# Performance work log

Measured on AMD Instinct MI355X. Metric: run time of the kernel, lower is better.

The kernel has to match this reference:

```python
import jax, jax.numpy as jnp
import numpy as np

B, L_TEXT, N_TOKEN = 8, 2048, 2048
C_TEXT, C_OUT = 3584, 384
C_HID = C_OUT * 2
CHAIN_TYPES = (1, 2)   # heavy, light
CDR_TYPES = (2, 4, 6)  # CDR1/2/3


def setup_inputs() -> dict:
    key = jax.random.key(0)
    ks = jax.random.split(key, 10)
    text_conditioning = jax.random.normal(ks[0], (B, L_TEXT, C_TEXT), jnp.float32)
    text_mask = jnp.ones((B, L_TEXT), jnp.int32)
    chain_type_ids = jax.random.randint(ks[1], (B, L_TEXT), 0, 3).astype(jnp.int32)
    cdr_region_type_ids = jax.random.randint(ks[2], (B, L_TEXT), 0, 10).astype(jnp.int32)
    boltz_chain_type = jax.random.randint(ks[3], (B, N_TOKEN), 0, 4).astype(jnp.int32)
    boltz_region_type = jax.random.randint(ks[4], (B, N_TOKEN), 0, 10).astype(jnp.int32)
    W1 = jax.random.normal(ks[5], (C_HID, C_TEXT), jnp.float32) * 0.02
    b1 = jnp.zeros((C_HID,), jnp.float32)
    W2 = jax.random.normal(ks[6], (C_OUT, C_HID), jnp.float32) * 0.02
    b2 = jnp.zeros((C_OUT,), jnp.float32)
    scale = jnp.ones((1,), jnp.float32)
    return {
        "text_conditioning": text_conditioning, "text_mask": text_mask,
        "chain_type_ids": chain_type_ids, "cdr_region_type_ids": cdr_region_type_ids,
        "boltz_chain_type": boltz_chain_type, "boltz_region_type": boltz_region_type,
        "W1": W1, "b1": b1, "W2": W2, "b2": b2, "scale": scale,
    }


def _align_one(text_proj, tmask, pmask):
    # text_proj: [L, C]; tmask: [L] bool (text CDR positions); pmask: [N] bool (protein CDR positions)
    # The k-th masked text token (in sequence order) maps to the k-th masked protein token,
    # for k < min(n_text, n_protein). Other protein positions get zeros.
    L = tmask.shape[0]
    trank = jnp.cumsum(tmask) - 1          # rank among text CDR tokens
    n_text = jnp.sum(tmask)
    prank = jnp.cumsum(pmask) - 1          # rank among protein CDR tokens
    # idx_by_rank[r] = text index whose rank is r; out-of-range scatter indices dropped
    idx_by_rank = jnp.zeros((L,), jnp.int32).at[jnp.where(tmask, trank, L)].set(
        jnp.arange(L, dtype=jnp.int32), mode="drop")
    valid = pmask & (prank < n_text)       # prank < n_protein holds by construction under pmask
    src = idx_by_rank[jnp.clip(prank, 0, L - 1)]
    emb = text_proj[src]                   # [N, C]
    return jnp.where(valid[:, None], emb, jnp.zeros((), text_proj.dtype))


def reference(text_conditioning, text_mask, chain_type_ids, cdr_region_type_ids,
              boltz_chain_type, boltz_region_type, W1, b1, W2, b2, scale):
    # 2-layer MLP projection: c_text -> 2*c_out -> c_out with SiLU
    h = jax.nn.silu(jnp.einsum("blt,ht->blh", text_conditioning, W1) + b1)
    text_proj = jnp.einsum("blh,ch->blc", h, W2) + b2    # [B, L, C_OUT]

    tm = text_mask.astype(bool)
    result = jnp.zeros((text_conditioning.shape[0], boltz_chain_type.shape[1], W2.shape[0]),
                       text_proj.dtype)
    align = jax.vmap(_align_one)
    for ct in CHAIN_TYPES:
        for rt in CDR_TYPES:
            tmask = (chain_type_ids == ct) & (cdr_region_type_ids == rt) & tm
            pmask = (boltz_chain_type == ct) & (boltz_region_type == rt)
            # (chain, cdr) pairs write to disjoint protein positions, so add is exact
            result = result + align(text_proj, tmask, pmask)
    return scale * result
```

## Files before the change

### kernel.cpp

```cpp
#include <hip/hip_runtime.h>
#include <hip/hip_bf16.h>
#include <math.h>

typedef __bf16 bf16_t;
typedef bf16_t bf16x8 __attribute__((ext_vector_type(8)));
typedef bf16_t bf16x4 __attribute__((ext_vector_type(4)));
typedef float f32x4 __attribute__((ext_vector_type(4)));

#define L_TEXT 2048
#define N_TOKEN 2048
#define C_TEXT 3584
#define C_OUT 384
#define C_HID 768
#define BATCH 8
#define MAXROWS (BATCH * N_TOKEN)
#define PM 3072
#define NPAIR (BATCH * 6)
#define KSPLIT 4
#define KCHUNK (C_TEXT / KSPLIT)

#define NW1 (C_HID * C_TEXT / 8)
#define NW2 (C_OUT * C_HID / 8)
#define NZERO (MAXROWS * C_OUT / 4)
#define CHUNKS_TOTAL (NW1 + NW2 + NZERO)
#define CHUNK_BLOCKS (CHUNKS_TOTAL / 256)
#define GCH (C_TEXT / 8)

__global__ __launch_bounds__(64) void scan_kernel(
    const int* __restrict__ tm, const int* __restrict__ ctid,
    const int* __restrict__ cdrid, const int* __restrict__ bct,
    const int* __restrict__ brt,
    int* __restrict__ trowL, int* __restrict__ pidxL, int* __restrict__ vcnt) {
    const int bp = blockIdx.x;
    const int lane = threadIdx.x;
    const int b = bp / 6, p = bp % 6;
    const int ct = (p < 3) ? 1 : 2;
    const int rt = 2 + 2 * (p % 3);
    const unsigned long long ltm = (1ull << lane) - 1ull;

    unsigned int tbits = 0, pbits = 0;
#pragma unroll
    for (int i = 0; i < 32; i++) {
        int l = i * 64 + lane;
        unsigned int m = (ctid[b * L_TEXT + l] == ct) &&
                         (cdrid[b * L_TEXT + l] == rt) &&
                         (tm[b * L_TEXT + l] != 0);
        tbits |= m << i;
    }
#pragma unroll
    for (int i = 0; i < 32; i++) {
        int n = i * 64 + lane;
        unsigned int m = (bct[b * N_TOKEN + n] == ct) &&
                         (brt[b * N_TOKEN + n] == rt);
        pbits |= m << i;
    }
    int base = 0;
#pragma unroll
    for (int i = 0; i < 32; i++) {
        bool m = (tbits >> i) & 1;
        unsigned long long bal = __ballot(m);
        if (m) trowL[bp * L_TEXT + base + __popcll(bal & ltm)] = i * 64 + lane;
        base += __popcll(bal);
    }
    const int n_text = base;
    base = 0;
#pragma unroll
    for (int i = 0; i < 32; i++) {
        bool m = (pbits >> i) & 1;
        unsigned long long bal = __ballot(m);
        if (m) pidxL[bp * L_TEXT + base + __popcll(bal & ltm)] = i * 64 + lane;
        base += __popcll(bal);
    }
    const int n_prot = base;
    if (lane == 0) vcnt[bp] = n_text < n_prot ? n_text : n_prot;
}

__global__ __launch_bounds__(256) void prep_kernel(
    const float* __restrict__ W1, const float* __restrict__ W2,
    bf16_t* __restrict__ W1b, bf16_t* __restrict__ W2b,
    float* __restrict__ outp,
    const float* __restrict__ X,
    const int* __restrict__ trowL, const int* __restrict__ pidxL,
    const int* __restrict__ vcnt,
    int* __restrict__ rows_dst, int* __restrict__ count,
    bf16_t* __restrict__ Xg) {
    const int t = threadIdx.x;
    if (blockIdx.x < CHUNK_BLOCKS) {
        int idx = blockIdx.x * 256 + t;
        if (idx < NW1) {
            int i = idx * 8;
            float4 v0 = *(const float4*)(W1 + i);
            float4 v1 = *(const float4*)(W1 + i + 4);
            bf16x8 o;
            o[0] = (bf16_t)v0.x; o[1] = (bf16_t)v0.y; o[2] = (bf16_t)v0.z; o[3] = (bf16_t)v0.w;
            o[4] = (bf16_t)v1.x; o[5] = (bf16_t)v1.y; o[6] = (bf16_t)v1.z; o[7] = (bf16_t)v1.w;
            *(bf16x8*)(W1b + i) = o;
        } else if (idx < NW1 + NW2) {
            int i = (idx - NW1) * 8;
            float4 v0 = *(const float4*)(W2 + i);
            float4 v1 = *(const float4*)(W2 + i + 4);
            bf16x8 o;
            o[0] = (bf16_t)v0.x; o[1] = (bf16_t)v0.y; o[2] = (bf16_t)v0.z; o[3] = (bf16_t)v0.w;
            o[4] = (bf16_t)v1.x; o[5] = (bf16_t)v1.y; o[6] = (bf16_t)v1.z; o[7] = (bf16_t)v1.w;
            *(bf16x8*)(W2b + i) = o;
        } else {
            int z = idx - NW1 - NW2;
            f32x4 zv = (f32x4){0.f, 0.f, 0.f, 0.f};
            *(f32x4*)(outp + (size_t)z * 4) = zv;
        }
        return;
    }

    __shared__ int vc[NPAIR];
    const int m = blockIdx.x - CHUNK_BLOCKS;
    if (t < NPAIR) vc[t] = vcnt[t];
    __syncthreads();

    int base = 0, bp = -1, total = 0;
    for (int q = 0; q < NPAIR; q++) {
        int v = vc[q];
        if (bp < 0 && m < base + v) bp = q;
        if (bp < 0) base += v;
        total += v;
    }
    if (m == 0 && t == 0) *count = total < PM ? total : PM;
    if (bp < 0 || m >= PM) return;
    const int r = m - base;
    const int b = bp / 6;

    if (t == 0) rows_dst[m] = b * N_TOKEN + pidxL[bp * L_TEXT + r];

    const int src = b * L_TEXT + trowL[bp * L_TEXT + r];
    const float* s = X + (size_t)src * C_TEXT;
    bf16_t* d = Xg + (size_t)m * C_TEXT;
    for (int c = t; c < GCH; c += 256) {
        int i = c * 8;
        float4 v0 = *(const float4*)(s + i);
        float4 v1 = *(const float4*)(s + i + 4);
        bf16x8 o;
        o[0] = (bf16_t)v0.x; o[1] = (bf16_t)v0.y; o[2] = (bf16_t)v0.z; o[3] = (bf16_t)v0.w;
        o[4] = (bf16_t)v1.x; o[5] = (bf16_t)v1.y; o[6] = (bf16_t)v1.z; o[7] = (bf16_t)v1.w;
        *(bf16x8*)(d + i) = o;
    }
}

__global__ __launch_bounds__(256) void gemm1_kernel(
    const bf16_t* __restrict__ Xg, const bf16_t* __restrict__ W1b,
    const int* __restrict__ countp, float* __restrict__ P) {
    int count = *countp; if (count > PM) count = PM;
    const int m0 = blockIdx.x * 128;
    if (m0 >= count) return;
    const int n0 = blockIdx.y * 128;
    const int kbeg = blockIdx.z * KCHUNK;

    __shared__ __align__(16) bf16_t As[2][128][40];
    __shared__ __align__(16) bf16_t Bs[2][128][40];

    const int t = threadIdx.x;
    const int lane = t & 63;
    const int w = t >> 6;
    const int wr = w >> 1, wc = w & 1;
    const int fr = lane & 15;
    const int kq = (lane >> 4) * 8;

    f32x4 acc[4][4];
#pragma unroll
    for (int i = 0; i < 4; i++)
#pragma unroll
        for (int j = 0; j < 4; j++) acc[i][j] = (f32x4){0.f, 0.f, 0.f, 0.f};

    const bf16_t* ap[2];
    const bf16_t* bp[2];
    int ofs[2];
#pragma unroll
    for (int j = 0; j < 2; j++) {
        int c = t + 256 * j;
        int row = c >> 2, c8 = (c & 3) * 8;
        ap[j] = Xg + (size_t)(m0 + row) * C_TEXT + kbeg + c8;
        bp[j] = W1b + (size_t)(n0 + row) * C_TEXT + kbeg + c8;
        ofs[j] = row * 40 + c8;
    }

    bf16_t* AsF = &As[0][0][0];
    bf16_t* BsF = &Bs[0][0][0];
    const int BUF = 128 * 40;

    bf16x8 ra[2], rb[2];
#pragma unroll
    for (int j = 0; j < 2; j++) { ra[j] = *(const bf16x8*)(ap[j]); rb[j] = *(const bf16x8*)(bp[j]); }

    const int T = KCHUNK / 32;
    for (int tile = 0; tile < T; ++tile) {
        const int cur = tile & 1;
#pragma unroll
        for (int j = 0; j < 2; j++) {
            *(bf16x8*)(AsF + cur * BUF + ofs[j]) = ra[j];
            *(bf16x8*)(BsF + cur * BUF + ofs[j]) = rb[j];
        }
        bf16x8 na[2], nb[2];
        bool more = (tile + 1 < T);
        if (more) {
            int k = (tile + 1) * 32;
#pragma unroll
            for (int j = 0; j < 2; j++) {
                na[j] = *(const bf16x8*)(ap[j] + k);
                nb[j] = *(const bf16x8*)(bp[j] + k);
            }
        }
        __syncthreads();
        bf16x8 af[4], bfr[4];
#pragma unroll
        for (int mi = 0; mi < 4; mi++)
            af[mi] = *(const bf16x8*)(AsF + cur * BUF + (wr * 64 + mi * 16 + fr) * 40 + kq);
#pragma unroll
        for (int ni = 0; ni < 4; ni++)
            bfr[ni] = *(const bf16x8*)(BsF + cur * BUF + (wc * 64 + ni * 16 + fr) * 40 + kq);
#pragma unroll
        for (int mi = 0; mi < 4; mi++)
#pragma unroll
            for (int ni = 0; ni < 4; ni++)
                acc[mi][ni] = __builtin_amdgcn_mfma_f32_16x16x32_bf16(
                    af[mi], bfr[ni], acc[mi][ni], 0, 0, 0);
        if (more) {
#pragma unroll
            for (int j = 0; j < 2; j++) { ra[j] = na[j]; rb[j] = nb[j]; }
        }
    }

    float* Pk = P + (size_t)blockIdx.z * PM * C_HID;
    const int rj = (lane >> 4) * 4;
#pragma unroll
    for (int mi = 0; mi < 4; mi++) {
#pragma unroll
        for (int ni = 0; ni < 4; ni++) {
            int gn = n0 + wc * 64 + ni * 16 + fr;
#pragma unroll
            for (int j = 0; j < 4; j++) {
                int gm = m0 + wr * 64 + mi * 16 + rj + j;
                if (gm < count) Pk[(size_t)gm * C_HID + gn] = acc[mi][ni][j];
            }
        }
    }
}

__global__ __launch_bounds__(256) void reduce1_kernel(
    const float* __restrict__ P, const float* __restrict__ b1,
    const int* __restrict__ countp, bf16_t* __restrict__ H) {
    int count = *countp; if (count > PM) count = PM;
    int idx = blockIdx.x * 256 + threadIdx.x;
    int m = idx / (C_HID / 4);
    int c = (idx % (C_HID / 4)) * 4;
    if (m >= count) return;
    f32x4 s = *(const f32x4*)(P + (size_t)m * C_HID + c);
#pragma unroll
    for (int ks = 1; ks < KSPLIT; ks++)
        s += *(const f32x4*)(P + ((size_t)ks * PM + m) * C_HID + c);
    f32x4 bb = *(const f32x4*)(b1 + c);
    bf16x4 o;
#pragma unroll
    for (int j = 0; j < 4; j++) {
        float v = s[j] + bb[j];
        o[j] = (bf16_t)(v / (1.0f + __expf(-v)));
    }
    *(bf16x4*)(H + (size_t)m * C_HID + c) = o;
}

__global__ __launch_bounds__(256) void gemm2_kernel(
    const bf16_t* __restrict__ Hm, const bf16_t* __restrict__ W2b,
    const float* __restrict__ b2, const int* __restrict__ rows_dst,
    const int* __restrict__ countp, const float* __restrict__ scale,
    float* __restrict__ outp) {
    int count = *countp; if (count > PM) count = PM;
    const int m0 = blockIdx.x * 32;
    if (m0 >= count) return;
    const int n0 = blockIdx.y * 128;

    __shared__ __align__(16) bf16_t As[2][32][40];
    __shared__ __align__(16) bf16_t Bs[2][128][40];

    const int t = threadIdx.x;
    const int lane = t & 63;
    const int w = t >> 6;
    const int fr = lane & 15;
    const int kq = (lane >> 4) * 8;

    f32x4 acc[2][2];
#pragma unroll
    for (int i = 0; i < 2; i++)
#pragma unroll
        for (int j = 0; j < 2; j++) acc[i][j] = (f32x4){0.f, 0.f, 0.f, 0.f};

    const int arow = t >> 2, ac8 = (t & 3) * 8;
    const bool astage = (t < 128);
    const bf16_t* ap = Hm + (size_t)(m0 + arow) * C_HID + ac8;
    const int aofs = arow * 40 + ac8;
    const bf16_t* bp[2];
    int bofs[2];
#pragma unroll
    for (int j = 0; j < 2; j++) {
        int c = t + 256 * j;
        int row = c >> 2, c8 = (c & 3) * 8;
        bp[j] = W2b + (size_t)(n0 + row) * C_HID + c8;
        bofs[j] = row * 40 + c8;
    }

    bf16_t* AsF = &As[0][0][0];
    bf16_t* BsF = &Bs[0][0][0];
    const int ABUF = 32 * 40, BBUF = 128 * 40;

    bf16x8 ra;
    if (astage) ra = *(const bf16x8*)(ap);
    bf16x8 rb0 = *(const bf16x8*)(bp[0]);
    bf16x8 rb1 = *(const bf16x8*)(bp[1]);

    const int T = C_HID / 32;
    for (int tile = 0; tile < T; ++tile) {
        const int cur = tile & 1;
        if (astage) *(bf16x8*)(AsF + cur * ABUF + aofs) = ra;
        *(bf16x8*)(BsF + cur * BBUF + bofs[0]) = rb0;
        *(bf16x8*)(BsF + cur * BBUF + bofs[1]) = rb1;
        bf16x8 na, nb0, nb1;
        bool more = (tile + 1 < T);
        if (more) {
            int k = (tile + 1) * 32;
            if (astage) na = *(const bf16x8*)(ap + k);
            nb0 = *(const bf16x8*)(bp[0] + k);
            nb1 = *(const bf16x8*)(bp[1] + k);
        }
        __syncthreads();
        bf16x8 af[2], bfr[2];
#pragma unroll
        for (int mi = 0; mi < 2; mi++)
            af[mi] = *(const bf16x8*)(AsF + cur * ABUF + (mi * 16 + fr) * 40 + kq);
#pragma unroll
        for (int ni = 0; ni < 2; ni++)
            bfr[ni] = *(const bf16x8*)(BsF + cur * BBUF + (w * 32 + ni * 16 + fr) * 40 + kq);
#pragma unroll
        for (int mi = 0; mi < 2; mi++)
#pragma unroll
            for (int ni = 0; ni < 2; ni++)
                acc[mi][ni] = __builtin_amdgcn_mfma_f32_16x16x32_bf16(
                    af[mi], bfr[ni], acc[mi][ni], 0, 0, 0);
        if (more) { if (astage) ra = na; rb0 = nb0; rb1 = nb1; }
        __syncthreads();
    }

    const float sc = scale[0];
    const int rj = (lane >> 4) * 4;
#pragma unroll
    for (int mi = 0; mi < 2; mi++) {
#pragma unroll
        for (int ni = 0; ni < 2; ni++) {
            int gn = n0 + w * 32 + ni * 16 + fr;
            float bias = b2[gn];
#pragma unroll
            for (int j = 0; j < 4; j++) {
                int gm = m0 + mi * 16 + rj + j;
                if (gm < count) {
                    int dst = rows_dst[gm];
                    outp[(size_t)dst * C_OUT + gn] = sc * (acc[mi][ni][j] + bias);
                }
            }
        }
    }
}

extern "C" void kernel_launch(void* const* d_in, const int* in_sizes, int n_in,
                              void* d_out, int out_size, void* d_ws, size_t ws_size,
                              hipStream_t stream) {
    const float* X     = (const float*)d_in[0];
    const int*   tm    = (const int*)d_in[1];
    const int*   ctid  = (const int*)d_in[2];
    const int*   cdrid = (const int*)d_in[3];
    const int*   bct   = (const int*)d_in[4];
    const int*   brt   = (const int*)d_in[5];
    const float* W1    = (const float*)d_in[6];
    const float* b1    = (const float*)d_in[7];
    const float* W2    = (const float*)d_in[8];
    const float* b2    = (const float*)d_in[9];
    const float* scale = (const float*)d_in[10];

    char* ws = (char*)d_ws;
    size_t off = 0;
    int* count = (int*)(ws + off);        off += 1024;
    int* vcnt = (int*)(ws + off);         off += 1024;
    int* rows_dst = (int*)(ws + off);     off += (size_t)PM * 4;
    int* trowL = (int*)(ws + off);        off += (size_t)NPAIR * L_TEXT * 4;
    int* pidxL = (int*)(ws + off);        off += (size_t)NPAIR * L_TEXT * 4;
    bf16_t* W1b = (bf16_t*)(ws + off);    off += (size_t)C_HID * C_TEXT * 2;
    bf16_t* W2b = (bf16_t*)(ws + off);    off += (size_t)C_OUT * C_HID * 2;
    bf16_t* Xg = (bf16_t*)(ws + off);     off += (size_t)PM * C_TEXT * 2;
    bf16_t* H = (bf16_t*)(ws + off);      off += (size_t)PM * C_HID * 2;
    float* P = (float*)(ws + off);        off += (size_t)KSPLIT * PM * C_HID * 4;
    float* outp = (float*)d_out;

    scan_kernel<<<NPAIR, 64, 0, stream>>>(tm, ctid, cdrid, bct, brt,
                                          trowL, pidxL, vcnt);

    prep_kernel<<<CHUNK_BLOCKS + PM, 256, 0, stream>>>(
        W1, W2, W1b, W2b, outp, X, trowL, pidxL, vcnt, rows_dst, count, Xg);

    dim3 g1(PM / 128, C_HID / 128, KSPLIT);
    gemm1_kernel<<<g1, 256, 0, stream>>>(Xg, W1b, count, P);

    reduce1_kernel<<<(PM * C_HID / 4) / 256, 256, 0, stream>>>(P, b1, count, H);

    dim3 g2(PM / 32, C_OUT / 128);
    gemm2_kernel<<<g2, 256, 0, stream>>>(H, W2b, b2, rows_dst, count, scale, outp);
}
```

Measured before the change: 124.0 us.

## Shrink gemm1 M-tile to 32 rows and halve K-split

```diff
diff --git a/kernel.cpp b/kernel.cpp
--- a/kernel.cpp
+++ b/kernel.cpp
@@ -16,7 +16,7 @@
 #define MAXROWS (BATCH * N_TOKEN)
 #define PM 3072
 #define NPAIR (BATCH * 6)
-#define KSPLIT 4
+#define KSPLIT 2
 #define KCHUNK (C_TEXT / KSPLIT)
 
 #define NW1 (C_HID * C_TEXT / 8)
@@ -148,95 +148,91 @@
     const bf16_t* __restrict__ Xg, const bf16_t* __restrict__ W1b,
     const int* __restrict__ countp, float* __restrict__ P) {
     int count = *countp; if (count > PM) count = PM;
-    const int m0 = blockIdx.x * 128;
+    const int m0 = blockIdx.x * 32;
     if (m0 >= count) return;
     const int n0 = blockIdx.y * 128;
     const int kbeg = blockIdx.z * KCHUNK;
 
-    __shared__ __align__(16) bf16_t As[2][128][40];
+    __shared__ __align__(16) bf16_t As[2][32][40];
     __shared__ __align__(16) bf16_t Bs[2][128][40];
 
     const int t = threadIdx.x;
     const int lane = t & 63;
     const int w = t >> 6;
-    const int wr = w >> 1, wc = w & 1;
     const int fr = lane & 15;
     const int kq = (lane >> 4) * 8;
 
-    f32x4 acc[4][4];
-#pragma unroll
-    for (int i = 0; i < 4; i++)
-#pragma unroll
-        for (int j = 0; j < 4; j++) acc[i][j] = (f32x4){0.f, 0.f, 0.f, 0.f};
-
-    const bf16_t* ap[2];
+    f32x4 acc[2][2];
+#pragma unroll
+    for (int i = 0; i < 2; i++)
+#pragma unroll
+        for (int j = 0; j < 2; j++) acc[i][j] = (f32x4){0.f, 0.f, 0.f, 0.f};
+
+    const int arow = t >> 2, ac8 = (t & 3) * 8;
+    const bool astage = (t < 128);
+    const bf16_t* ap = Xg + (size_t)(m0 + arow) * C_TEXT + kbeg + ac8;
+    const int aofs = arow * 40 + ac8;
     const bf16_t* bp[2];
-    int ofs[2];
+    int bofs[2];
 #pragma unroll
     for (int j = 0; j < 2; j++) {
         int c = t + 256 * j;
         int row = c >> 2, c8 = (c & 3) * 8;
-        ap[j] = Xg + (size_t)(m0 + row) * C_TEXT + kbeg + c8;
         bp[j] = W1b + (size_t)(n0 + row) * C_TEXT + kbeg + c8;
-        ofs[j] = row * 40 + c8;
+        bofs[j] = row * 40 + c8;
     }
 
     bf16_t* AsF = &As[0][0][0];
     bf16_t* BsF = &Bs[0][0][0];
-    const int BUF = 128 * 40;
-
-    bf16x8 ra[2], rb[2];
-#pragma unroll
-    for (int j = 0; j < 2; j++) { ra[j] = *(const bf16x8*)(ap[j]); rb[j] = *(const bf16x8*)(bp[j]); }
+    const int ABUF = 32 * 40, BBUF = 128 * 40;
+
+    bf16x8 ra;
+    if (astage) ra = *(const bf16x8*)(ap);
+    bf16x8 rb0 = *(const bf16x8*)(bp[0]);
+    bf16x8 rb1 = *(const bf16x8*)(bp[1]);
 
     const int T = KCHUNK / 32;
     for (int tile = 0; tile < T; ++tile) {
         const int cur = tile & 1;
-#pragma unroll
-        for (int j = 0; j < 2; j++) {
-            *(bf16x8*)(AsF + cur * BUF + ofs[j]) = ra[j];
-            *(bf16x8*)(BsF + cur * BUF + ofs[j]) = rb[j];
-        }
-        bf16x8 na[2], nb[2];
+        if (astage) *(bf16x8*)(AsF + cur * ABUF + aofs) = ra;
+        *(bf16x8*)(BsF + cur * BBUF + bofs[0]) = rb0;
+        *(bf16x8*)(BsF + cur * BBUF + bofs[1]) = rb1;
+        bf16x8 na, nb0, nb1;
         bool more = (tile + 1 < T);
         if (more) {
             int k = (tile + 1) * 32;
-#pragma unroll
-            for (int j = 0; j < 2; j++) {
-                na[j] = *(const bf16x8*)(ap[j] + k);
-                nb[j] = *(const bf16x8*)(bp[j] + k);
-            }
+            if (astage) na = *(const bf16x8*)(ap + k);
+            nb0 = *(const bf16x8*)(bp[0] + k);
+            nb1 = *(const bf16x8*)(bp[1] + k);
         }
         __syncthreads();
-        bf16x8 af[4], bfr[4];
-#pragma unroll
-        for (int mi = 0; mi < 4; mi++)
-            af[mi] = *(const bf16x8*)(AsF + cur * BUF + (wr * 64 + mi * 16 + fr) * 40 + kq);
-#pragma unroll
-        for (int ni = 0; ni < 4; ni++)
-            bfr[ni] = *(const bf16x8*)(BsF + cur * BUF + (wc * 64 + ni * 16 + fr) * 40 + kq);
-#pragma unroll
-        for (int mi = 0; mi < 4; mi++)
-#pragma unroll
-            for (int ni = 0; ni < 4; ni++)
+        bf16x8 af[2], bfr[2];
+#pragma unroll
+        for (int mi = 0; mi < 2; mi++)
+            af[mi] = *(const bf16x8*)(AsF + cur * ABUF + (mi * 16 + fr) * 40 + kq);
+#pragma unroll
+        for (int ni = 0; ni < 2; ni++)
+            bfr[ni] = *(const bf16x8*)(BsF + cur * BBUF + (w * 32 + ni * 16 + fr) * 40 + kq);
+#pragma unroll
+        for (int mi = 0; mi < 2; mi++)
+#pragma unroll
+            for (int ni = 0; ni < 2; ni++)
                 acc[mi][ni] = __builtin_amdgcn_mfma_f32_16x16x32_bf16(
                     af[mi], bfr[ni], acc[mi][ni], 0, 0, 0);
-        if (more) {
-#pragma unroll
-            for (int j = 0; j < 2; j++) { ra[j] = na[j]; rb[j] = nb[j]; }
-        }
+        if (more) { if (astage) ra = na; rb0 = nb0; rb1 = nb1; }
+        __syncthreads();
     }
 
     float* Pk = P + (size_t)blockIdx.z * PM * C_HID;
     const int rj = (lane >> 4) * 4;
 #pragma unroll
-    for (int mi = 0; mi < 4; mi++) {
-#pragma unroll
-        for (int ni = 0; ni < 4; ni++) {
-            int gn = n0 + wc * 64 + ni * 16 + fr;
+    for (int mi = 0; mi < 2; mi++) {
+#pragma unroll
+        for (int ni = 0; ni < 2; ni++) {
+            int gn = n0 + w * 32 + ni * 16 + fr;
 #pragma unroll
             for (int j = 0; j < 4; j++) {
-                int gm = m0 + wr * 64 + mi * 16 + rj + j;
+                int gm = m0 + mi * 16 + rj + j;
                 if (gm < count) Pk[(size_t)gm * C_HID + gn] = acc[mi][ni][j];
             }
         }
@@ -400,7 +396,7 @@
     prep_kernel<<<CHUNK_BLOCKS + PM, 256, 0, stream>>>(
         W1, W2, W1b, W2b, outp, X, trowL, pidxL, vcnt, rows_dst, count, Xg);
 
-    dim3 g1(PM / 128, C_HID / 128, KSPLIT);
+    dim3 g1(PM / 32, C_HID / 128, KSPLIT);
     gemm1_kernel<<<g1, 256, 0, stream>>>(Xg, W1b, count, P);
 
     reduce1_kernel<<<(PM * C_HID / 4) / 256, 256, 0, stream>>>(P, b1, count, H);
```

Result: slower. 137.0 us (+10.5%).
